# Performance work log

Measured on AMD Instinct MI355X. Metric: run time of the kernel, lower is better.

## Reference

```python
import jax, jax.numpy as jnp
import numpy as np

N, A, B, H = 16, 2048, 2048, 64


def setup_inputs() -> dict:
    key = jax.random.key(0)
    k1, k2, k3, k4 = jax.random.split(key, 4)
    query = jax.random.normal(k1, (N, A, H), dtype=jnp.float32)
    key_t = jax.random.normal(k2, (N, B, H), dtype=jnp.float32)
    value = jax.random.normal(k3, (N, B, H), dtype=jnp.float32)
    mask = jax.random.randint(k4, (N, B), 0, 2).astype(bool)  # True = masked out
    return {"query": query, "key": key_t, "value": value, "mask": mask}


def reference(query, key, value, mask):
    # attention_product: scaled dot product -> (n, a, b) logits
    h = query.shape[-1]
    scale = 1.0 / jnp.sqrt(jnp.asarray(h, dtype=query.dtype))
    logit = jnp.einsum("nah,nbh->nab", query, key) * scale
    # mask (n, b) broadcast over query axis; masked positions -> -inf
    logit = jnp.where(mask[:, None, :], -jnp.inf, logit)
    attn = jax.nn.softmax(logit, axis=-1)
    # dropout_rate = 0.0 (eval) -> identity
    context = jnp.einsum("nab,nbh->nah", attn, value)
    return context
```

## Files before the change

kernel.cpp:

```cpp
#include <hip/hip_runtime.h>

#define NB 16
#define AQ 2048
#define BKV 2048
#define HD 64

#define L2E 1.44269504f
#define QSCALE 0.18033688f
#define MBIAS -43000.0f

typedef float f32x4 __attribute__((ext_vector_type(4)));
typedef float f32x16 __attribute__((ext_vector_type(16)));
typedef short bf16x8 __attribute__((ext_vector_type(8)));
typedef int int4v __attribute__((ext_vector_type(4)));

__device__ __forceinline__ short f2bf(float f) {
  return __builtin_bit_cast(short, static_cast<__bf16>(f));
}
__device__ __forceinline__ unsigned pk2(float a, float b) {
  unsigned lo = (unsigned short)f2bf(a);
  unsigned hh = (unsigned short)f2bf(b);
  return lo | (hh << 16);
}

__global__ __launch_bounds__(256) void prepack(const float* __restrict__ K,
                                               const float* __restrict__ V,
                                               short* __restrict__ Kb,
                                               short* __restrict__ Vt) {
  if (blockIdx.x < 1024) {
    size_t base = ((size_t)blockIdx.x * 256 + threadIdx.x) * 8;
    f32x4 a = *(const f32x4*)(K + base);
    f32x4 b = *(const f32x4*)(K + base + 4);
    bf16x8 o;
#pragma unroll
    for (int i = 0; i < 4; ++i) {
      o[i] = f2bf(a[i]);
      o[i + 4] = f2bf(b[i]);
    }
    *(bf16x8*)(Kb + base) = o;
  } else {
    unsigned vb = blockIdx.x - 1024;
    int n = vb >> 5;
    int b0 = (vb & 31) * 64;
    int t = threadIdx.x;
    __shared__ short tile[64][68];
    int rb = t >> 4;
    int hc = (t & 15) * 4;
#pragma unroll
    for (int j = 0; j < 4; ++j) {
      int r = rb + 16 * j;
      f32x4 v = *(const f32x4*)(V + ((size_t)n * BKV + b0 + r) * HD + hc);
#pragma unroll
      for (int i = 0; i < 4; ++i) tile[r][hc + i] = f2bf(v[i]);
    }
    __syncthreads();
    int hr = t >> 2;
    int bb = (t & 3) * 16;
    bf16x8 o0, o1;
#pragma unroll
    for (int j = 0; j < 8; ++j) {
      o0[j] = tile[bb + j][hr];
      o1[j] = tile[bb + 8 + j][hr];
    }
    short* dst = Vt + ((size_t)n * HD + hr) * BKV + b0 + bb;
    *(bf16x8*)dst = o0;
    *(bf16x8*)(dst + 8) = o1;
  }
}

template <int PRE>
__global__ __launch_bounds__(256, 2) void attn_fwd(
    const float* __restrict__ Q, const float* __restrict__ K,
    const float* __restrict__ V, const int* __restrict__ M,
    const short* __restrict__ Kb, const short* __restrict__ Vt,
    float* __restrict__ O) {
  unsigned orig = blockIdx.x;
  unsigned wg = (orig & 7u) * 64u + (orig >> 3);
  int n = (int)(wg >> 5);
  int q0 = (int)(wg & 31u) * 64;

  int w = threadIdx.x >> 6;
  int lane = threadIdx.x & 63;
  int hi = lane >> 5;
  int li = lane & 31;
  int qg = w >> 1;
  int half = w & 1;
  int q0w = q0 + qg * 32;

  const float* Qn = Q + (size_t)n * AQ * HD;
  const float* Kn = K + (size_t)n * BKV * HD;
  const float* Vn = V + (size_t)n * BKV * HD;
  const short* Kbn = Kb + (size_t)n * BKV * HD;
  const short* Vtn = Vt + (size_t)n * HD * BKV;
  const int* Mn = M + (size_t)n * BKV;

  __shared__ __align__(16) float pacc[4][32][68];
  __shared__ float Ml[4][2][32];

  bf16x8 qb[4];
#pragma unroll
  for (int ks = 0; ks < 4; ++ks) {
    const float* qp = Qn + (size_t)(q0w + li) * HD + 16 * ks + 8 * hi;
    f32x4 a = *(const f32x4*)qp;
    f32x4 b = *(const f32x4*)(qp + 4);
#pragma unroll
    for (int i = 0; i < 4; ++i) {
      qb[ks][i] = f2bf(a[i] * QSCALE);
      qb[ks][i + 4] = f2bf(b[i] * QSCALE);
    }
  }

  f32x16 acc0 = {};
  f32x16 acc1 = {};
  float m_run = -1e30f;
  float l_run = 0.f;

  const int bstart = half * (BKV / 2);
  for (int b0 = bstart; b0 < bstart + (BKV / 2); b0 += 32) {
    int4v mv[4];
#pragma unroll
    for (int j = 0; j < 4; ++j)
      mv[j] = *(const int4v*)(Mn + b0 + 8 * j + 4 * hi);
    f32x16 st;
#pragma unroll
    for (int j = 0; j < 4; ++j)
#pragma unroll
      for (int r = 0; r < 4; ++r) st[4 * j + r] = mv[j][r] ? MBIAS : 0.f;

#pragma unroll
    for (int ks = 0; ks < 4; ++ks) {
      bf16x8 ka;
      if constexpr (PRE) {
        ka = *(const bf16x8*)(Kbn + (size_t)(b0 + li) * HD + 16 * ks + 8 * hi);
      } else {
        const float* kp = Kn + (size_t)(b0 + li) * HD + 16 * ks + 8 * hi;
        f32x4 k0 = *(const f32x4*)kp;
        f32x4 k1 = *(const f32x4*)(kp + 4);
#pragma unroll
        for (int i = 0; i < 4; ++i) {
          ka[i] = f2bf(k0[i]);
          ka[i + 4] = f2bf(k1[i]);
        }
      }
      st = __builtin_amdgcn_mfma_f32_32x32x16_bf16(ka, qb[ks], st, 0, 0, 0);
    }

    float mt = st[0];
#pragma unroll
    for (int i = 1; i < 16; ++i) mt = fmaxf(mt, st[i]);
    mt = fmaxf(mt, __shfl_xor(mt, 32));
    float m_new = fmaxf(m_run, mt);
    float fac = exp2f(m_run - m_new);

    float rs = 0.f;
#pragma unroll
    for (int i = 0; i < 16; ++i) {
      float e = exp2f(st[i] - m_new);
      st[i] = e;
      rs += e;
    }
    rs += __shfl_xor(rs, 32);
    l_run = l_run * fac + rs;
    m_run = m_new;

#pragma unroll
    for (int i = 0; i < 16; ++i) {
      acc0[i] *= fac;
      acc1[i] *= fac;
    }

    unsigned w8[8], sx[8];
#pragma unroll
    for (int j = 0; j < 8; ++j) w8[j] = pk2(st[2 * j], st[2 * j + 1]);
#pragma unroll
    for (int j = 0; j < 8; ++j) sx[j] = (unsigned)__shfl_xor((int)w8[j], 32);
    int4v p0 = {(int)(hi ? sx[2] : w8[0]), (int)(hi ? sx[3] : w8[1]),
                (int)(hi ? w8[2] : sx[0]), (int)(hi ? w8[3] : sx[1])};
    int4v p1 = {(int)(hi ? sx[6] : w8[4]), (int)(hi ? sx[7] : w8[5]),
                (int)(hi ? w8[6] : sx[4]), (int)(hi ? w8[7] : sx[5])};
    bf16x8 pb0 = __builtin_bit_cast(bf16x8, p0);
    bf16x8 pb1 = __builtin_bit_cast(bf16x8, p1);

#pragma unroll
    for (int ht = 0; ht < 2; ++ht) {
      bf16x8 va0, va1;
      if constexpr (PRE) {
        const short* vp = Vtn + (size_t)(32 * ht + li) * BKV + b0 + 8 * hi;
        va0 = *(const bf16x8*)vp;
        va1 = *(const bf16x8*)(vp + 16);
      } else {
#pragma unroll
        for (int j = 0; j < 8; ++j) {
          va0[j] = f2bf(Vn[(size_t)(b0 + 8 * hi + j) * HD + 32 * ht + li]);
          va1[j] = f2bf(Vn[(size_t)(b0 + 16 + 8 * hi + j) * HD + 32 * ht + li]);
        }
      }
      if (ht == 0) {
        acc0 = __builtin_amdgcn_mfma_f32_32x32x16_bf16(va0, pb0, acc0, 0, 0, 0);
        acc0 = __builtin_amdgcn_mfma_f32_32x32x16_bf16(va1, pb1, acc0, 0, 0, 0);
      } else {
        acc1 = __builtin_amdgcn_mfma_f32_32x32x16_bf16(va0, pb0, acc1, 0, 0, 0);
        acc1 = __builtin_amdgcn_mfma_f32_32x32x16_bf16(va1, pb1, acc1, 0, 0, 0);
      }
    }
  }

  if (hi == 0) {
    Ml[w][0][li] = m_run;
    Ml[w][1][li] = l_run;
  }
#pragma unroll
  for (int reg = 0; reg < 16; ++reg) {
    int hrow = (reg & 3) + 8 * (reg >> 2) + 4 * hi;
    pacc[w][li][hrow] = acc0[reg];
    pacc[w][li][32 + hrow] = acc1[reg];
  }
  __syncthreads();

  {
    int tid = threadIdx.x;
    int q = tid >> 2;
    int qg2 = q >> 5;
    int ql = q & 31;
    int hb = (tid & 3) * 16;
    float ma = Ml[qg2 * 2 + 0][0][ql], mb = Ml[qg2 * 2 + 1][0][ql];
    float mmax = fmaxf(ma, mb);
    float fa = exp2f(ma - mmax), fb = exp2f(mb - mmax);
    float l = fa * Ml[qg2 * 2 + 0][1][ql] + fb * Ml[qg2 * 2 + 1][1][ql];
    float inv = 1.0f / l;
    float* op = O + ((size_t)n * AQ + q0 + q) * HD + hb;
#pragma unroll
    for (int t = 0; t < 4; ++t) {
      f32x4 xa = *(const f32x4*)&pacc[qg2 * 2 + 0][ql][hb + 4 * t];
      f32x4 xb = *(const f32x4*)&pacc[qg2 * 2 + 1][ql][hb + 4 * t];
      f32x4 res;
#pragma unroll
      for (int i = 0; i < 4; ++i) res[i] = (fa * xa[i] + fb * xb[i]) * inv;
      *(f32x4*)(op + 4 * t) = res;
    }
  }
}

extern "C" void kernel_launch(void* const* d_in, const int* in_sizes, int n_in,
                              void* d_out, int out_size, void* d_ws, size_t ws_size,
                              hipStream_t stream) {
  const float* q = (const float*)d_in[0];
  const float* k = (const float*)d_in[1];
  const float* v = (const float*)d_in[2];
  const int* m = (const int*)d_in[3];
  float* o = (float*)d_out;

  const size_t kv_elems = (size_t)NB * BKV * HD;
  const size_t need = kv_elems * 2 * sizeof(short);

  if (ws_size >= need) {
    short* kb = (short*)d_ws;
    short* vt = kb + kv_elems;
    prepack<<<dim3(1536), dim3(256), 0, stream>>>(k, v, kb, vt);
    attn_fwd<1><<<dim3(NB * (AQ / 64)), dim3(256), 0, stream>>>(q, k, v, m, kb, vt, o);
  } else {
    attn_fwd<0><<<dim3(NB * (AQ / 64)), dim3(256), 0, stream>>>(q, k, v, m, nullptr, nullptr, o);
  }
}
```

Measured before the change: 147.0 us.

## Split KV across four waves per 32-query block to double grid size

Each workgroup now handles 32 queries, with all four waves working on the same queries but on different quarters of the key/value sequence. The epilogue merges four partial softmax states instead of two. This doubles the number of workgroups and raises the launch-bound occupancy target to improve CU utilisation and latency hiding. The trade-off is more K/V traffic per query (K/V is re-read by twice as many blocks) and a larger cross-wave reduction.

```diff
diff --git a/kernel.cpp b/kernel.cpp
--- a/kernel.cpp
+++ b/kernel.cpp
@@ -5,7 +5,6 @@
 #define BKV 2048
 #define HD 64
 
-#define L2E 1.44269504f
 #define QSCALE 0.18033688f
 #define MBIAS -43000.0f
 
@@ -69,23 +68,20 @@
 }
 
 template <int PRE>
-__global__ __launch_bounds__(256, 2) void attn_fwd(
+__global__ __launch_bounds__(256, 4) void attn_fwd(
     const float* __restrict__ Q, const float* __restrict__ K,
     const float* __restrict__ V, const int* __restrict__ M,
     const short* __restrict__ Kb, const short* __restrict__ Vt,
     float* __restrict__ O) {
   unsigned orig = blockIdx.x;
-  unsigned wg = (orig & 7u) * 64u + (orig >> 3);
-  int n = (int)(wg >> 5);
-  int q0 = (int)(wg & 31u) * 64;
+  unsigned wg = (orig & 7u) * 128u + (orig >> 3);
+  int n = (int)(wg >> 6);
+  int q0 = (int)(wg & 63u) * 32;
 
   int w = threadIdx.x >> 6;
   int lane = threadIdx.x & 63;
   int hi = lane >> 5;
   int li = lane & 31;
-  int qg = w >> 1;
-  int half = w & 1;
-  int q0w = q0 + qg * 32;
 
   const float* Qn = Q + (size_t)n * AQ * HD;
   const float* Kn = K + (size_t)n * BKV * HD;
@@ -100,7 +96,7 @@
   bf16x8 qb[4];
 #pragma unroll
   for (int ks = 0; ks < 4; ++ks) {
-    const float* qp = Qn + (size_t)(q0w + li) * HD + 16 * ks + 8 * hi;
+    const float* qp = Qn + (size_t)(q0 + li) * HD + 16 * ks + 8 * hi;
     f32x4 a = *(const f32x4*)qp;
     f32x4 b = *(const f32x4*)(qp + 4);
 #pragma unroll
@@ -115,8 +111,8 @@
   float m_run = -1e30f;
   float l_run = 0.f;
 
-  const int bstart = half * (BKV / 2);
-  for (int b0 = bstart; b0 < bstart + (BKV / 2); b0 += 32) {
+  const int bstart = w * (BKV / 4);
+  for (int b0 = bstart; b0 < bstart + (BKV / 4); b0 += 32) {
     int4v mv[4];
 #pragma unroll
     for (int j = 0; j < 4; ++j)
@@ -219,23 +215,29 @@
 
   {
     int tid = threadIdx.x;
-    int q = tid >> 2;
-    int qg2 = q >> 5;
-    int ql = q & 31;
-    int hb = (tid & 3) * 16;
-    float ma = Ml[qg2 * 2 + 0][0][ql], mb = Ml[qg2 * 2 + 1][0][ql];
-    float mmax = fmaxf(ma, mb);
-    float fa = exp2f(ma - mmax), fb = exp2f(mb - mmax);
-    float l = fa * Ml[qg2 * 2 + 0][1][ql] + fb * Ml[qg2 * 2 + 1][1][ql];
+    int q = tid >> 3;
+    int hb = (tid & 7) * 8;
+    float m0 = Ml[0][0][q], m1 = Ml[1][0][q];
+    float m2 = Ml[2][0][q], m3 = Ml[3][0][q];
+    float mmax = fmaxf(fmaxf(m0, m1), fmaxf(m2, m3));
+    float f[4] = {exp2f(m0 - mmax), exp2f(m1 - mmax), exp2f(m2 - mmax),
+                  exp2f(m3 - mmax)};
+    float l = f[0] * Ml[0][1][q] + f[1] * Ml[1][1][q] + f[2] * Ml[2][1][q] +
+              f[3] * Ml[3][1][q];
     float inv = 1.0f / l;
     float* op = O + ((size_t)n * AQ + q0 + q) * HD + hb;
 #pragma unroll
-    for (int t = 0; t < 4; ++t) {
-      f32x4 xa = *(const f32x4*)&pacc[qg2 * 2 + 0][ql][hb + 4 * t];
-      f32x4 xb = *(const f32x4*)&pacc[qg2 * 2 + 1][ql][hb + 4 * t];
+    for (int t = 0; t < 2; ++t) {
+      f32x4 o = {0.f, 0.f, 0.f, 0.f};
+#pragma unroll
+      for (int ww = 0; ww < 4; ++ww) {
+        f32x4 a = *(const f32x4*)&pacc[ww][q][hb + 4 * t];
+#pragma unroll
+        for (int i = 0; i < 4; ++i) o[i] += f[ww] * a[i];
+      }
       f32x4 res;
 #pragma unroll
-      for (int i = 0; i < 4; ++i) res[i] = (fa * xa[i] + fb * xb[i]) * inv;
+      for (int i = 0; i < 4; ++i) res[i] = o[i] * inv;
       *(f32x4*)(op + 4 * t) = res;
     }
   }
@@ -257,8 +259,8 @@
     short* kb = (short*)d_ws;
     short* vt = kb + kv_elems;
     prepack<<<dim3(1536), dim3(256), 0, stream>>>(k, v, kb, vt);
-    attn_fwd<1><<<dim3(NB * (AQ / 64)), dim3(256), 0, stream>>>(q, k, v, m, kb, vt, o);
+    attn_fwd<1><<<dim3(NB * (AQ / 32)), dim3(256), 0, stream>>>(q, k, v, m, kb, vt, o);
   } else {
-    attn_fwd<0><<<dim3(NB * (AQ / 64)), dim3(256), 0, stream>>>(q, k, v, m, nullptr, nullptr, o);
-  }
-}
+    attn_fwd<0><<<dim3(NB * (AQ / 32)), dim3(256), 0, stream>>>(q, k, v, m, nullptr, nullptr, o);
+  }
+}
```

Result: no change. 148.6 us (+1.1%).
